# Kernel tuning notes

Measured on AMD Instinct MI355X. Metric: run time of the kernel, lower is better.

The kernel has to match this reference:

```python
import jax, jax.numpy as jnp
import numpy as np

B, S, H, D = 1, 2048, 32, 128
HID = H * D
ROPE_BASE = 10000.0
NEG = -1e9  # finite large-negative for causal mask (avoids NaNs in grads)


def permute_w(W, head_dim):
    """permute_W from the module: per head, interleave first/second half rows."""
    r = W.reshape(-1, head_dim, W.shape[-1])            # (H, D, in)
    half = head_dim // 2
    out = jnp.stack([r[:, :half], r[:, half:]], axis=2)  # (H, D/2, 2, in)
    return out.reshape(W.shape)


def rotate_half(x):
    """Interleaved rotate: even dims <- -odd, odd dims <- even."""
    x2 = x.reshape(x.shape[:-1] + (-1, 2))
    return jnp.stack([-x2[..., 1], x2[..., 0]], axis=-1).reshape(x.shape)


def setup_inputs() -> dict:
    key = jax.random.key(0)
    ks = jax.random.split(key, 6)
    scale = 0.02
    hidden_states = jax.random.normal(ks[0], (B, S, HID), jnp.float32)
    Wq = jax.random.normal(ks[1], (HID, HID), jnp.float32) * scale
    Wk = jax.random.normal(ks[2], (HID, HID), jnp.float32) * scale
    Wv = jax.random.normal(ks[3], (HID, HID), jnp.float32) * scale
    Wo = jax.random.normal(ks[4], (HID, HID), jnp.float32) * scale
    # additive causal mask [B,1,S,S]
    causal = jnp.tril(jnp.ones((S, S), dtype=bool))
    attention_mask = jnp.where(causal, 0.0, NEG).astype(jnp.float32)[None, None]
    position_ids = jnp.arange(S, dtype=jnp.int64)[None]  # [B,S]
    return dict(hidden_states=hidden_states, attention_mask=attention_mask,
                Wq=Wq, Wk=Wk, Wv=Wv, Wo=Wo, position_ids=position_ids)


def reference(hidden_states, attention_mask, Wq, Wk, Wv, Wo, position_ids):
    bsz, q_len, _ = hidden_states.shape
    # init-time weight permutation (norm2 == 1 since do_calc=False)
    Wqp = permute_w(Wq, D)
    Wkp = permute_w(Wk, D)

    q = (hidden_states @ Wqp.T).reshape(bsz, q_len, H, D).transpose(0, 2, 1, 3)
    k = (hidden_states @ Wkp.T).reshape(bsz, q_len, H, D).transpose(0, 2, 1, 3)
    v = (hidden_states @ Wv.T).reshape(bsz, q_len, H, D).transpose(0, 2, 1, 3)

    # interleaved RoPE cache: emb = repeat_interleave(freqs, 2)
    inv_freq = 1.0 / (ROPE_BASE ** (jnp.arange(0, D, 2, dtype=jnp.float32) / D))
    t = jnp.arange(q_len, dtype=jnp.float32)
    emb = jnp.repeat(jnp.outer(t, inv_freq), 2, axis=-1)          # [S, D]
    cos = jnp.cos(emb)[position_ids][:, None]                     # [B,1,S,D]
    sin = jnp.sin(emb)[position_ids][:, None]
    q = q * cos + rotate_half(q) * sin
    k = k * cos + rotate_half(k) * sin

    scores = jnp.einsum('bhqd,bhkd->bhqk', q, k) / jnp.sqrt(jnp.float32(D))
    scores = scores + attention_mask
    probs = jax.nn.softmax(scores.astype(jnp.float32), axis=-1).astype(q.dtype)
    attn = jnp.einsum('bhqk,bhkd->bhqd', probs, v)
    attn = attn.transpose(0, 2, 1, 3).reshape(bsz, q_len, HID)
    return attn @ Wo.T
```

## Files before the change

kernel.cpp:

```cpp
#include <hip/hip_runtime.h>
#include <hip/hip_bf16.h>
#include <stdint.h>

#define S_LEN 2048
#define NHEAD 32
#define DHEAD 128
#define HID 4096

typedef __bf16 bf16x8 __attribute__((ext_vector_type(8)));
typedef float f32x4 __attribute__((ext_vector_type(4)));

__device__ inline void glds16(const void* g, void* l) {
  __builtin_amdgcn_global_load_lds(
      (const __attribute__((address_space(1))) void*)(uintptr_t)g,
      (__attribute__((address_space(3))) void*)(uint32_t)(uintptr_t)l,
      16, 0, 0);
}

__global__ void cast_plain(const float* __restrict__ in, __bf16* __restrict__ out, int n) {
  int i = (blockIdx.x * 256 + threadIdx.x) * 8;
  if (i >= n) return;
  bf16x8 r;
#pragma unroll
  for (int j = 0; j < 8; ++j) r[j] = (__bf16)in[i + j];
  *(bf16x8*)(out + i) = r;
}

__global__ void cast_permute(const float* __restrict__ in, __bf16* __restrict__ out) {
  int i = (blockIdx.x * 256 + threadIdx.x) * 8;
  int row = i >> 12;
  int col = i & 4095;
  int d = row & 127;
  int src = (row & ~127) + ((d & 1) ? 64 + (d >> 1) : (d >> 1));
  const float* p = in + (size_t)src * HID + col;
  bf16x8 r;
#pragma unroll
  for (int j = 0; j < 8; ++j) r[j] = (__bf16)p[j];
  *(bf16x8*)(out + i) = r;
}

template <bool F32OUT>
__global__ __launch_bounds__(256, 2) void gemm_bt(const __bf16* __restrict__ A,
                                                  const __bf16* __restrict__ B,
                                                  void* __restrict__ Cv,
                                                  int M, int N, int K) {
  __shared__ __align__(16) __bf16 As[128 * 64];
  __shared__ __align__(16) __bf16 Bs[128 * 64];
  const int t = threadIdx.x;
  const int w = t >> 6, lane = t & 63;
  const int l15 = lane & 15, lg = lane >> 4;
  const int brow = blockIdx.y * 128, bcol = blockIdx.x * 128;
  const int wr = (w >> 1) * 64, wc = (w & 1) * 64;

  const f32x4 zero = {0.f, 0.f, 0.f, 0.f};
  f32x4 acc[4][4];
#pragma unroll
  for (int i = 0; i < 4; ++i)
#pragma unroll
    for (int j = 0; j < 4; ++j) acc[i][j] = zero;

  const int rstage = t >> 3;
  const int cstage = (t & 7) * 8;
  const __bf16* Ag = A + (size_t)(brow + rstage) * K + cstage;
  const __bf16* Bg = B + (size_t)(bcol + rstage) * K + cstage;

  for (int k0 = 0; k0 < K; k0 += 64) {
#pragma unroll
    for (int i = 0; i < 4; ++i) {
      glds16(Ag + (size_t)(i * 32) * K, &As[i * 2048 + w * 512]);
      glds16(Bg + (size_t)(i * 32) * K, &Bs[i * 2048 + w * 512]);
    }
    Ag += 64;
    Bg += 64;
    asm volatile("s_waitcnt vmcnt(0)" ::: "memory");
    __syncthreads();
#pragma unroll
    for (int kk = 0; kk < 2; ++kk) {
      bf16x8 a[4], b[4];
      const int ko = kk * 32 + lg * 8;
#pragma unroll
      for (int i = 0; i < 4; ++i)
        a[i] = *(const bf16x8*)&As[(wr + i * 16 + l15) * 64 + ko];
#pragma unroll
      for (int j = 0; j < 4; ++j)
        b[j] = *(const bf16x8*)&Bs[(wc + j * 16 + l15) * 64 + ko];
#pragma unroll
      for (int i = 0; i < 4; ++i)
#pragma unroll
        for (int j = 0; j < 4; ++j)
          acc[i][j] = __builtin_amdgcn_mfma_f32_16x16x32_bf16(a[i], b[j], acc[i][j], 0, 0, 0);
    }
    __syncthreads();
  }

#pragma unroll
  for (int i = 0; i < 4; ++i)
#pragma unroll
    for (int j = 0; j < 4; ++j)
#pragma unroll
      for (int r = 0; r < 4; ++r) {
        int row = brow + wr + i * 16 + lg * 4 + r;
        int col = bcol + wc + j * 16 + l15;
        if (F32OUT)
          ((float*)Cv)[(size_t)row * N + col] = acc[i][j][r];
        else
          ((__bf16*)Cv)[(size_t)row * N + col] = (__bf16)acc[i][j][r];
      }
}

__global__ void rope_kernel(__bf16* __restrict__ X) {
  int idx = (blockIdx.x * 256 + threadIdx.x) * 8;
  int srow = idx >> 12;
  int d = idx & 127;
  float tpos = (float)srow;
  bf16x8 v = *(const bf16x8*)(X + idx);
  float f[8];
#pragma unroll
  for (int j = 0; j < 8; ++j) f[j] = (float)v[j];
#pragma unroll
  for (int p = 0; p < 4; ++p) {
    int i = (d >> 1) + p;
    float ang = tpos * exp2f(-0.20762050593046014f * (float)i);
    float sn, cs;
    sincosf(ang, &sn, &cs);
    float e = f[2 * p], o = f[2 * p + 1];
    f[2 * p] = e * cs - o * sn;
    f[2 * p + 1] = o * cs + e * sn;
  }
#pragma unroll
  for (int j = 0; j < 8; ++j) v[j] = (__bf16)f[j];
  *(bf16x8*)(X + idx) = v;
}

__global__ void transpose_v(const __bf16* __restrict__ v, __bf16* __restrict__ vt) {
  __shared__ __bf16 tile[32][33];
  int x = blockIdx.x * 32 + threadIdx.x;
  int y0 = blockIdx.y * 32;
  for (int j = threadIdx.y; j < 32; j += 8)
    tile[j][threadIdx.x] = v[(size_t)(y0 + j) * HID + x];
  __syncthreads();
  for (int j = threadIdx.y; j < 32; j += 8)
    vt[(size_t)(blockIdx.x * 32 + j) * S_LEN + y0 + threadIdx.x] = tile[threadIdx.x][j];
}

__global__ __launch_bounds__(256, 1) void attn_kernel(const __bf16* __restrict__ Q,
                                                      const __bf16* __restrict__ K,
                                                      const __bf16* __restrict__ Vt,
                                                      __bf16* __restrict__ O) {
  __shared__ __align__(16) __bf16 Ks[2][64 * 128];
  __shared__ __align__(16) __bf16 Vs[2][128 * 64];
  __shared__ __align__(16) __bf16 Ps[4][32 * 64];
  const int t = threadIdx.x, w = t >> 6, lane = t & 63;
  const int l15 = lane & 15, lg = lane >> 4;
  const int b = blockIdx.x;
  const int h = b & 31;
  const int x = b >> 5;
  const float scale = 0.08838834764831845f;

  auto stage = [&](int buf, int kv0) {
#pragma unroll
    for (int i = 0; i < 4; ++i) {
      int le = i * 2048 + t * 8;
      int row = le >> 7, colel = le & 127;
      int sc = colel ^ ((row & 7) << 3);
      glds16(K + (size_t)(kv0 + row) * HID + h * 128 + sc, &Ks[buf][le]);
    }
#pragma unroll
    for (int i = 0; i < 4; ++i) {
      int le = i * 2048 + t * 8;
      int row = le >> 6, colel = le & 63;
      int sc = colel ^ ((row & 7) << 3);
      glds16(Vt + (size_t)(h * 128 + row) * S_LEN + kv0 + sc, &Vs[buf][le]);
    }
  };

  const f32x4 zero = {0.f, 0.f, 0.f, 0.f};

#pragma unroll 1
  for (int ti = 0; ti < 2; ++ti) {
    const int qt = ti ? (15 - x) : x;
    const int r0 = qt * 128 + w * 32;

    bf16x8 qf[2][4];
#pragma unroll
    for (int g = 0; g < 2; ++g)
#pragma unroll
      for (int kk = 0; kk < 4; ++kk)
        qf[g][kk] = *(const bf16x8*)&Q[(size_t)(r0 + g * 16 + l15) * HID + h * 128 + kk * 32 + lg * 8];

    f32x4 o[2][8];
    float m[2][4], lsum[2][4];
#pragma unroll
    for (int g = 0; g < 2; ++g) {
#pragma unroll
      for (int n = 0; n < 8; ++n) o[g][n] = zero;
#pragma unroll
      for (int r = 0; r < 4; ++r) { m[g][r] = -1e30f; lsum[g][r] = 0.f; }
    }

    const int nt = 2 * qt + 2;
    __syncthreads();
    stage(0, 0);

#pragma unroll 1
    for (int j = 0; j < nt; ++j) {
      const int kv0 = j * 64;
      const int buf = j & 1;
      asm volatile("s_waitcnt vmcnt(0)" ::: "memory");
      __syncthreads();
      if (j + 1 < nt) stage(buf ^ 1, kv0 + 64);

      f32x4 s[2][4];
#pragma unroll
      for (int g = 0; g < 2; ++g)
#pragma unroll
        for (int tt = 0; tt < 4; ++tt) s[g][tt] = zero;
#pragma unroll
      for (int kk = 0; kk < 4; ++kk)
#pragma unroll
        for (int tt = 0; tt < 4; ++tt) {
          const int krow = tt * 16 + l15;
          bf16x8 kf = *(const bf16x8*)&Ks[buf][krow * 128 + ((kk * 32 + lg * 8) ^ ((krow & 7) << 3))];
          s[0][tt] = __builtin_amdgcn_mfma_f32_16x16x32_bf16(qf[0][kk], kf, s[0][tt], 0, 0, 0);
          s[1][tt] = __builtin_amdgcn_mfma_f32_16x16x32_bf16(qf[1][kk], kf, s[1][tt], 0, 0, 0);
        }

      const bool domask = (j >= 2 * qt);
#pragma unroll
      for (int g = 0; g < 2; ++g)
#pragma unroll
        for (int r = 0; r < 4; ++r) {
          const int row = r0 + g * 16 + lg * 4 + r;
          float v[4];
#pragma unroll
          for (int tt = 0; tt < 4; ++tt) {
            v[tt] = s[g][tt][r] * scale;
            if (domask) v[tt] += ((kv0 + tt * 16 + l15) <= row) ? 0.f : -1e9f;
          }
          float mx = fmaxf(fmaxf(v[0], v[1]), fmaxf(v[2], v[3]));
#pragma unroll
          for (int off = 1; off < 16; off <<= 1) mx = fmaxf(mx, __shfl_xor(mx, off));
          float mn = fmaxf(m[g][r], mx);
          float sc_ = __expf(m[g][r] - mn);
          m[g][r] = mn;
          float rs = 0.f;
          const int lrow = g * 16 + lg * 4 + r;
#pragma unroll
          for (int tt = 0; tt < 4; ++tt) {
            float p = __expf(v[tt] - mn);
            rs += p;
            const int col = tt * 16 + l15;
            Ps[w][lrow * 64 + (col ^ ((lrow & 7) << 3))] = (__bf16)p;
          }
#pragma unroll
          for (int off = 1; off < 16; off <<= 1) rs += __shfl_xor(rs, off);
          lsum[g][r] = lsum[g][r] * sc_ + rs;
#pragma unroll
          for (int n = 0; n < 8; ++n) o[g][n][r] *= sc_;
        }

      asm volatile("s_waitcnt lgkmcnt(0)" ::: "memory");
#pragma unroll
      for (int c = 0; c < 2; ++c) {
        const int cb = c * 32 + lg * 8;
        bf16x8 pa0 = *(const bf16x8*)&Ps[w][l15 * 64 + (cb ^ ((l15 & 7) << 3))];
        bf16x8 pa1 = *(const bf16x8*)&Ps[w][(16 + l15) * 64 + (cb ^ ((l15 & 7) << 3))];
#pragma unroll
        for (int n = 0; n < 8; ++n) {
          const int vrow = n * 16 + l15;
          bf16x8 vbf = *(const bf16x8*)&Vs[buf][vrow * 64 + (cb ^ ((vrow & 7) << 3))];
          o[0][n] = __builtin_amdgcn_mfma_f32_16x16x32_bf16(pa0, vbf, o[0][n], 0, 0, 0);
          o[1][n] = __builtin_amdgcn_mfma_f32_16x16x32_bf16(pa1, vbf, o[1][n], 0, 0, 0);
        }
      }
    }

#pragma unroll
    for (int g = 0; g < 2; ++g)
#pragma unroll
      for (int r = 0; r < 4; ++r) {
        const float inv = 1.f / lsum[g][r];
        const int row = r0 + g * 16 + lg * 4 + r;
#pragma unroll
        for (int n = 0; n < 8; ++n)
          O[(size_t)row * HID + h * 128 + n * 16 + l15] = (__bf16)(o[g][n][r] * inv);
      }
  }
}

extern "C" void kernel_launch(void* const* d_in, const int* in_sizes, int n_in,
                              void* d_out, int out_size, void* d_ws, size_t ws_size,
                              hipStream_t stream) {
  const float* hs = (const float*)d_in[0];
  const float* Wq = (const float*)d_in[2];
  const float* Wk = (const float*)d_in[3];
  const float* Wv = (const float*)d_in[4];
  const float* Wo = (const float*)d_in[5];
  float* out = (float*)d_out;

  char* ws = (char*)d_ws;
  size_t off = 0;
  auto alloc = [&](size_t nbytes) {
    void* p = ws + off;
    off += (nbytes + 255) & ~(size_t)255;
    return p;
  };
  __bf16* hsb = (__bf16*)alloc((size_t)S_LEN * HID * 2);
  __bf16* wqb = (__bf16*)alloc((size_t)HID * HID * 2);
  __bf16* wkb = (__bf16*)alloc((size_t)HID * HID * 2);
  __bf16* wvb = (__bf16*)alloc((size_t)HID * HID * 2);
  __bf16* wob = (__bf16*)alloc((size_t)HID * HID * 2);
  __bf16* qb = (__bf16*)alloc((size_t)S_LEN * HID * 2);
  __bf16* kb = (__bf16*)alloc((size_t)S_LEN * HID * 2);
  __bf16* vb = (__bf16*)alloc((size_t)S_LEN * HID * 2);
  __bf16* vtb = (__bf16*)alloc((size_t)S_LEN * HID * 2);
  __bf16* ab = (__bf16*)alloc((size_t)S_LEN * HID * 2);

  cast_plain<<<S_LEN * HID / 8 / 256, 256, 0, stream>>>(hs, hsb, S_LEN * HID);
  cast_permute<<<HID * HID / 8 / 256, 256, 0, stream>>>(Wq, wqb);
  cast_permute<<<HID * HID / 8 / 256, 256, 0, stream>>>(Wk, wkb);
  cast_plain<<<HID * HID / 8 / 256, 256, 0, stream>>>(Wv, wvb, HID * HID);
  cast_plain<<<HID * HID / 8 / 256, 256, 0, stream>>>(Wo, wob, HID * HID);

  dim3 gg(HID / 128, S_LEN / 128);
  gemm_bt<false><<<gg, 256, 0, stream>>>(hsb, wqb, qb, S_LEN, HID, HID);
  gemm_bt<false><<<gg, 256, 0, stream>>>(hsb, wkb, kb, S_LEN, HID, HID);
  gemm_bt<false><<<gg, 256, 0, stream>>>(hsb, wvb, vb, S_LEN, HID, HID);

  rope_kernel<<<S_LEN * HID / 8 / 256, 256, 0, stream>>>(qb);
  rope_kernel<<<S_LEN * HID / 8 / 256, 256, 0, stream>>>(kb);

  transpose_v<<<dim3(HID / 32, S_LEN / 32), dim3(32, 8), 0, stream>>>(vb, vtb);

  attn_kernel<<<256, 256, 0, stream>>>(qb, kb, vtb, ab);

  gemm_bt<true><<<gg, 256, 0, stream>>>(ab, wob, out, S_LEN, HID, HID);
}
```

Measured before the change: 931.8 us.

## Replace GEMM with 256x256 double-buffered 8-wave pipeline and fuse QKV projections

Replaces the 128x128 single-buffered GEMM with a 256x256-tile, 512-thread kernel. It double-buffers LDS with staggered async global-to-LDS loads, uses XOR-swizzled LDS layout, raises MFMA priority with s_setprio, and remaps blocks so neighbouring tiles land on the same XCD. The Q, K and V weights are packed into one buffer so a single launch computes all three projections. s_setprio is also added around the attention MFMAs. It aims to hide memory latency behind MFMA and cut launch and L2 overhead, at the cost of 128KB LDS per block and tricky hand-written vmcnt accounting.

```diff
diff --git a/kernel.cpp b/kernel.cpp
--- a/kernel.cpp
+++ b/kernel.cpp
@@ -39,72 +39,134 @@
   *(bf16x8*)(out + i) = r;
 }
 
-template <bool F32OUT>
-__global__ __launch_bounds__(256, 2) void gemm_bt(const __bf16* __restrict__ A,
-                                                  const __bf16* __restrict__ B,
-                                                  void* __restrict__ Cv,
-                                                  int M, int N, int K) {
-  __shared__ __align__(16) __bf16 As[128 * 64];
-  __shared__ __align__(16) __bf16 Bs[128 * 64];
+#define PHASE(BUF, Q, LOADB, VM, ...)                                          \
+  do {                                                                         \
+    if (LOADB) {                                                               \
+      _Pragma("unroll") for (int n = 0; n < 4; ++n)                            \
+          _Pragma("unroll") for (int kk = 0; kk < 2; ++kk)                     \
+              bfr[n][kk] = dsB(BUF, n, kk);                                    \
+    }                                                                          \
+    _Pragma("unroll") for (int s = 0; s < 2; ++s)                              \
+        _Pragma("unroll") for (int kk = 0; kk < 2; ++kk)                       \
+            afr[s][kk] = dsA(BUF, 2 * (Q) + s, kk);                            \
+    __VA_ARGS__;                                                               \
+    if ((VM) == 1)                                                             \
+      asm volatile("s_waitcnt vmcnt(4)" ::: "memory");                         \
+    else if ((VM) == 2)                                                        \
+      asm volatile("s_waitcnt vmcnt(0)" ::: "memory");                         \
+    __builtin_amdgcn_s_barrier();                                              \
+    __builtin_amdgcn_s_setprio(1);                                             \
+    _Pragma("unroll") for (int kk = 0; kk < 2; ++kk)                           \
+        _Pragma("unroll") for (int s = 0; s < 2; ++s)                          \
+            _Pragma("unroll") for (int n = 0; n < 4; ++n)                      \
+                acc[2 * (Q) + s][n] = __builtin_amdgcn_mfma_f32_16x16x32_bf16( \
+                    afr[s][kk], bfr[n][kk], acc[2 * (Q) + s][n], 0, 0, 0);     \
+    __builtin_amdgcn_s_setprio(0);                                             \
+    __builtin_amdgcn_s_barrier();                                              \
+  } while (0)
+
+template <bool F32OUT, bool QKV>
+__global__ __launch_bounds__(512, 2) void gemm8p(const __bf16* __restrict__ A,
+                                                 const __bf16* __restrict__ B,
+                                                 void* __restrict__ C0,
+                                                 void* __restrict__ C1,
+                                                 void* __restrict__ C2,
+                                                 int NBX) {
+  __shared__ __align__(16) __bf16 sA[32768];
+  __shared__ __align__(16) __bf16 sB[32768];
   const int t = threadIdx.x;
-  const int w = t >> 6, lane = t & 63;
+  const int lane = t & 63;
   const int l15 = lane & 15, lg = lane >> 4;
-  const int brow = blockIdx.y * 128, bcol = blockIdx.x * 128;
-  const int wr = (w >> 1) * 64, wc = (w & 1) * 64;
-
+  const int wid = t >> 6;
+  const int wr = wid >> 2, wc = wid & 3;
+  const int K = 4096;
+
+  const int L = blockIdx.x;
+  const int xcd = L & 7, j = L >> 3;
+  const int by = j & 7;
+  const int bx = xcd * (NBX >> 3) + (j >> 3);
+  const int brow = by * 256, bcol = bx * 256;
+
+  const int srow = t >> 3;
+  const int gcol = (((t & 7) ^ (srow & 7)) << 3);
+  const int ldsoff = t * 8;
+
+  auto stageA = [&](int buf, int h, int kt) {
+    const __bf16* g = A + (size_t)(brow + h * 128 + srow) * K + kt * 64 + gcol;
+    __bf16* l = &sA[((buf * 2 + h) << 13) + ldsoff];
+    glds16(g, l);
+    glds16(g + (size_t)64 * K, l + 4096);
+  };
+  auto stageB = [&](int buf, int h, int kt) {
+    const __bf16* g = B + (size_t)(bcol + h * 128 + srow) * K + kt * 64 + gcol;
+    __bf16* l = &sB[((buf * 2 + h) << 13) + ldsoff];
+    glds16(g, l);
+    glds16(g + (size_t)64 * K, l + 4096);
+  };
+  auto dsA = [&](int buf, int m, int kk) -> bf16x8 {
+    return *(const bf16x8*)&sA[((buf * 2 + wr) << 13) + (m * 16 + l15) * 64 +
+                               ((((kk << 2) | lg) ^ (l15 & 7)) << 3)];
+  };
+  auto dsB = [&](int buf, int n, int kk) -> bf16x8 {
+    return *(const bf16x8*)&sB[((buf * 2 + (wc >> 1)) << 13) +
+                               ((wc & 1) * 64 + n * 16 + l15) * 64 +
+                               ((((kk << 2) | lg) ^ (l15 & 7)) << 3)];
+  };
+
+  f32x4 acc[8][4];
   const f32x4 zero = {0.f, 0.f, 0.f, 0.f};
-  f32x4 acc[4][4];
-#pragma unroll
-  for (int i = 0; i < 4; ++i)
-#pragma unroll
-    for (int j = 0; j < 4; ++j) acc[i][j] = zero;
-
-  const int rstage = t >> 3;
-  const int cstage = (t & 7) * 8;
-  const __bf16* Ag = A + (size_t)(brow + rstage) * K + cstage;
-  const __bf16* Bg = B + (size_t)(bcol + rstage) * K + cstage;
-
-  for (int k0 = 0; k0 < K; k0 += 64) {
-#pragma unroll
-    for (int i = 0; i < 4; ++i) {
-      glds16(Ag + (size_t)(i * 32) * K, &As[i * 2048 + w * 512]);
-      glds16(Bg + (size_t)(i * 32) * K, &Bs[i * 2048 + w * 512]);
-    }
-    Ag += 64;
-    Bg += 64;
-    asm volatile("s_waitcnt vmcnt(0)" ::: "memory");
-    __syncthreads();
-#pragma unroll
-    for (int kk = 0; kk < 2; ++kk) {
-      bf16x8 a[4], b[4];
-      const int ko = kk * 32 + lg * 8;
-#pragma unroll
-      for (int i = 0; i < 4; ++i)
-        a[i] = *(const bf16x8*)&As[(wr + i * 16 + l15) * 64 + ko];
-#pragma unroll
-      for (int j = 0; j < 4; ++j)
-        b[j] = *(const bf16x8*)&Bs[(wc + j * 16 + l15) * 64 + ko];
-#pragma unroll
-      for (int i = 0; i < 4; ++i)
-#pragma unroll
-        for (int j = 0; j < 4; ++j)
-          acc[i][j] = __builtin_amdgcn_mfma_f32_16x16x32_bf16(a[i], b[j], acc[i][j], 0, 0, 0);
-    }
-    __syncthreads();
+#pragma unroll
+  for (int m = 0; m < 8; ++m)
+#pragma unroll
+    for (int n = 0; n < 4; ++n) acc[m][n] = zero;
+  bf16x8 bfr[4][2], afr[2][2];
+
+  stageA(0, 0, 0);
+  stageA(0, 1, 0);
+  stageB(0, 0, 0);
+  stageB(0, 1, 0);
+  stageB(1, 0, 1);
+  stageB(1, 1, 1);
+  asm volatile("s_waitcnt vmcnt(4)" ::: "memory");
+  __builtin_amdgcn_s_barrier();
+
+#pragma unroll 1
+  for (int i = 0; i < 32; ++i) {
+    const int kt = 2 * i;
+    const bool last = (i == 31);
+    PHASE(0, 0, true, 0, { stageA(1, 0, kt + 1); stageA(1, 1, kt + 1); });
+    PHASE(0, 1, false, 0, { if (!last) stageB(0, 0, kt + 2); });
+    PHASE(0, 2, false, 0, { if (!last) stageB(0, 1, kt + 2); });
+    PHASE(0, 3, false, (last ? 2 : 1), {});
+    PHASE(1, 0, true, 0, { if (!last) stageA(0, 0, kt + 2); });
+    PHASE(1, 1, false, 0, { if (!last) stageA(0, 1, kt + 2); });
+    PHASE(1, 2, false, 0, { if (!last) stageB(1, 0, kt + 3); });
+    PHASE(1, 3, false, (last ? 2 : 1), { if (!last) stageB(1, 1, kt + 3); });
   }
 
-#pragma unroll
-  for (int i = 0; i < 4; ++i)
-#pragma unroll
-    for (int j = 0; j < 4; ++j)
-#pragma unroll
-      for (int r = 0; r < 4; ++r) {
-        int row = brow + wr + i * 16 + lg * 4 + r;
-        int col = bcol + wc + j * 16 + l15;
-        if (F32OUT)
-          ((float*)Cv)[(size_t)row * N + col] = acc[i][j][r];
+  void* Cbase;
+  int colbase;
+  if constexpr (QKV) {
+    const int sel = bcol >> 12;
+    Cbase = sel == 0 ? C0 : (sel == 1 ? C1 : C2);
+    colbase = (bcol & 4095) + wc * 64;
+  } else {
+    Cbase = C0;
+    colbase = bcol + wc * 64;
+  }
+  const int rowbase = brow + wr * 128;
+#pragma unroll
+  for (int m = 0; m < 8; ++m)
+#pragma unroll
+    for (int n = 0; n < 4; ++n)
+#pragma unroll
+      for (int rr = 0; rr < 4; ++rr) {
+        const int row = rowbase + m * 16 + lg * 4 + rr;
+        const int col = colbase + n * 16 + l15;
+        if constexpr (F32OUT)
+          ((float*)Cbase)[(size_t)row * 4096 + col] = acc[m][n][rr];
         else
-          ((__bf16*)Cv)[(size_t)row * N + col] = (__bf16)acc[i][j][r];
+          ((__bf16*)Cbase)[(size_t)row * 4096 + col] = (__bf16)acc[m][n][rr];
       }
 }
 
@@ -215,6 +277,7 @@
       for (int g = 0; g < 2; ++g)
 #pragma unroll
         for (int tt = 0; tt < 4; ++tt) s[g][tt] = zero;
+      __builtin_amdgcn_s_setprio(1);
 #pragma unroll
       for (int kk = 0; kk < 4; ++kk)
 #pragma unroll
@@ -224,6 +287,7 @@
           s[0][tt] = __builtin_amdgcn_mfma_f32_16x16x32_bf16(qf[0][kk], kf, s[0][tt], 0, 0, 0);
           s[1][tt] = __builtin_amdgcn_mfma_f32_16x16x32_bf16(qf[1][kk], kf, s[1][tt], 0, 0, 0);
         }
+      __builtin_amdgcn_s_setprio(0);
 
       const bool domask = (j >= 2 * qt);
 #pragma unroll
@@ -260,6 +324,7 @@
         }
 
       asm volatile("s_waitcnt lgkmcnt(0)" ::: "memory");
+      __builtin_amdgcn_s_setprio(1);
 #pragma unroll
       for (int c = 0; c < 2; ++c) {
         const int cb = c * 32 + lg * 8;
@@ -273,6 +338,7 @@
           o[1][n] = __builtin_amdgcn_mfma_f32_16x16x32_bf16(pa1, vbf, o[1][n], 0, 0, 0);
         }
       }
+      __builtin_amdgcn_s_setprio(0);
     }
 
 #pragma unroll
@@ -306,9 +372,7 @@
     return p;
   };
   __bf16* hsb = (__bf16*)alloc((size_t)S_LEN * HID * 2);
-  __bf16* wqb = (__bf16*)alloc((size_t)HID * HID * 2);
-  __bf16* wkb = (__bf16*)alloc((size_t)HID * HID * 2);
-  __bf16* wvb = (__bf16*)alloc((size_t)HID * HID * 2);
+  __bf16* wqkv = (__bf16*)alloc((size_t)3 * HID * HID * 2);
   __bf16* wob = (__bf16*)alloc((size_t)HID * HID * 2);
   __bf16* qb = (__bf16*)alloc((size_t)S_LEN * HID * 2);
   __bf16* kb = (__bf16*)alloc((size_t)S_LEN * HID * 2);
@@ -317,15 +381,12 @@
   __bf16* ab = (__bf16*)alloc((size_t)S_LEN * HID * 2);
 
   cast_plain<<<S_LEN * HID / 8 / 256, 256, 0, stream>>>(hs, hsb, S_LEN * HID);
-  cast_permute<<<HID * HID / 8 / 256, 256, 0, stream>>>(Wq, wqb);
-  cast_permute<<<HID * HID / 8 / 256, 256, 0, stream>>>(Wk, wkb);
-  cast_plain<<<HID * HID / 8 / 256, 256, 0, stream>>>(Wv, wvb, HID * HID);
+  cast_permute<<<HID * HID / 8 / 256, 256, 0, stream>>>(Wq, wqkv);
+  cast_permute<<<HID * HID / 8 / 256, 256, 0, stream>>>(Wk, wqkv + (size_t)HID * HID);
+  cast_plain<<<HID * HID / 8 / 256, 256, 0, stream>>>(Wv, wqkv + (size_t)2 * HID * HID, HID * HID);
   cast_plain<<<HID * HID / 8 / 256, 256, 0, stream>>>(Wo, wob, HID * HID);
 
-  dim3 gg(HID / 128, S_LEN / 128);
-  gemm_bt<false><<<gg, 256, 0, stream>>>(hsb, wqb, qb, S_LEN, HID, HID);
-  gemm_bt<false><<<gg, 256, 0, stream>>>(hsb, wkb, kb, S_LEN, HID, HID);
-  gemm_bt<false><<<gg, 256, 0, stream>>>(hsb, wvb, vb, S_LEN, HID, HID);
+  gemm8p<false, true><<<384, 512, 0, stream>>>(hsb, wqkv, qb, kb, vb, 48);
 
   rope_kernel<<<S_LEN * HID / 8 / 256, 256, 0, stream>>>(qb);
   rope_kernel<<<S_LEN * HID / 8 / 256, 256, 0, stream>>>(kb);
@@ -334,5 +395,5 @@
 
   attn_kernel<<<256, 256, 0, stream>>>(qb, kb, vtb, ab);
 
-  gemm_bt<true><<<gg, 256, 0, stream>>>(ab, wob, out, S_LEN, HID, HID);
-}
+  gemm8p<true, false><<<128, 512, 0, stream>>>(ab, wob, out, nullptr, nullptr, 16);
+}
```

Result: faster. 746.5 us (-19.9%).
